# Kernel optimization log

Hardware: AMD Instinct MI355X
Metric: run time of the kernel (lower is better)

Reference implementation:

```python
import jax, jax.numpy as jnp
import numpy as np

B, L, D, C, H, M = 256, 500, 3, 32, 512, 5
I = D + C            # per-step input dim (dihedrals concat condition)
O = D * M            # out_dim * num_mixtures


def setup_inputs() -> dict:
    key = jax.random.key(0)
    ks = jax.random.split(key, 6)
    return {
        "inputs": jax.random.normal(ks[0], (B, L, D), dtype=jnp.float32),
        "z": jax.random.normal(ks[1], (B, L, C), dtype=jnp.float32),
        "W_enc": jax.random.normal(ks[2], (L, I, H), dtype=jnp.float32),
        "b_enc": jnp.zeros((1, H), dtype=jnp.float32),
        "V_mu": jax.random.normal(ks[3], (L, H, O), dtype=jnp.float32),
        "b_mu": jnp.zeros((L, 1, O), dtype=jnp.float32),
        "V_sigma": jax.random.normal(ks[4], (L, H, O), dtype=jnp.float32),
        "b_sigma": jnp.zeros((L, 1, O), dtype=jnp.float32),
        "V_pi": jax.random.normal(ks[5], (L, H, M), dtype=jnp.float32),
        "b_pi": jnp.zeros((L, 1, M), dtype=jnp.float32),
    }


def reference(inputs, z, W_enc, b_enc, V_mu, b_mu, V_sigma, b_sigma, V_pi, b_pi):
    # x: [L, B, I]
    x = jnp.transpose(jnp.concatenate([inputs, z], axis=2), (1, 0, 2))
    # per-step contributions c[i] = x[i] @ W_enc[i] -> [L, B, H]
    c = jnp.einsum('lbi,lih->lbh', x, W_enc)
    # a[i] = b_enc + sum_{j<i} c[j]  (exclusive prefix sum of the recurrence)
    csum = jnp.cumsum(c, axis=0)
    a = jnp.concatenate([jnp.zeros_like(csum[:1]), csum[:-1]], axis=0) + b_enc
    h = jax.nn.relu(a)  # [L, B, H]
    h_mu = jnp.einsum('lbh,lho->lbo', h, V_mu) + b_mu        # [L, B, O]
    h_sigma = jnp.einsum('lbh,lho->lbo', h, V_sigma) + b_sigma
    h_pi = jnp.einsum('lbh,lhm->lbm', h, V_pi) + b_pi        # [L, B, M]
    logits = jnp.concatenate([h_mu, h_sigma, h_pi], axis=2)  # [L, B, 2O+M]
    return jnp.transpose(logits, (1, 0, 2))                  # [B, L, 2O+M]
```

## Files before the change

### kernel.cpp

```cpp
#include <hip/hip_runtime.h>

constexpr int B = 256, L = 500, D = 3, C = 32, I = 35, H = 512, O = 15, M = 5;
constexpr int KP1 = 48;
constexpr int JP = 48;
constexpr int KPV = 520;
constexpr int G = 100;
constexpr int LC = 5;

typedef __attribute__((ext_vector_type(8))) _Float16 half8;
typedef __attribute__((ext_vector_type(2))) _Float16 half2;
typedef __attribute__((ext_vector_type(16))) float f32x16;

__global__ __launch_bounds__(256) void k0x(const float* __restrict__ inp,
                                           const float* __restrict__ z,
                                           _Float16* __restrict__ xT) {
  const int l = blockIdx.x, tid = threadIdx.x;
  __shared__ _Float16 xs[B][38];
  const float* ip = inp + ((size_t)tid * L + l) * D;
  const float4* zp = (const float4*)(z + ((size_t)tid * L + l) * C);
  xs[tid][0] = (_Float16)ip[0];
  xs[tid][1] = (_Float16)ip[1];
  xs[tid][2] = (_Float16)ip[2];
#pragma unroll
  for (int q = 0; q < 8; ++q) {
    float4 v = zp[q];
    xs[tid][D + q * 4 + 0] = (_Float16)v.x;
    xs[tid][D + q * 4 + 1] = (_Float16)v.y;
    xs[tid][D + q * 4 + 2] = (_Float16)v.z;
    xs[tid][D + q * 4 + 3] = (_Float16)v.w;
  }
  __syncthreads();
  unsigned int* dst = (unsigned int*)(xT + (size_t)l * B * KP1);
  for (int f = tid; f < B * (KP1 / 2); f += 256) {
    int b = f / (KP1 / 2), k = (f - b * (KP1 / 2)) * 2;
    unsigned int lo = (k < I)     ? *(const unsigned short*)&xs[b][k]     : 0u;
    unsigned int hi = (k + 1 < I) ? *(const unsigned short*)&xs[b][k + 1] : 0u;
    dst[f] = lo | (hi << 16);
  }
}

__global__ __launch_bounds__(256) void k0w(const float* __restrict__ W,
                                           _Float16* __restrict__ Wt) {
  const int l = blockIdx.x, tid = threadIdx.x;
  __shared__ _Float16 ws[H][37];
  for (int f = tid; f < I * H; f += 256) {
    int i = f >> 9, h = f & 511;
    ws[h][i] = (_Float16)W[((size_t)l * I + i) * H + h];
  }
  __syncthreads();
  unsigned int* dst = (unsigned int*)(Wt + (size_t)l * H * KP1);
  for (int f = tid; f < H * (KP1 / 2); f += 256) {
    int h = f / (KP1 / 2), k = (f - h * (KP1 / 2)) * 2;
    unsigned int lo = (k < I)     ? *(const unsigned short*)&ws[h][k]     : 0u;
    unsigned int hi = (k + 1 < I) ? *(const unsigned short*)&ws[h][k + 1] : 0u;
    dst[f] = lo | (hi << 16);
  }
}

__global__ __launch_bounds__(256) void k0v(const float* __restrict__ Vmu,
                                           const float* __restrict__ Vsg,
                                           const float* __restrict__ Vpi,
                                           _Float16* __restrict__ Vt) {
  const int l = blockIdx.x, tid = threadIdx.x;
  __shared__ __align__(16) _Float16 Vs[JP * KPV];
  for (int f = tid; f < (JP * KPV) / 8; f += 256) ((uint4*)Vs)[f] = (uint4){0, 0, 0, 0};
  __syncthreads();
  const float* vm = Vmu + (size_t)l * H * O;
  const float* vs = Vsg + (size_t)l * H * O;
  const float* vp = Vpi + (size_t)l * H * M;
  for (int idx = tid; idx < H * O; idx += 256) {
    int k = idx / O, j = idx - k * O;
    Vs[j * KPV + k]       = (_Float16)vm[idx];
    Vs[(O + j) * KPV + k] = (_Float16)vs[idx];
  }
  for (int idx = tid; idx < H * M; idx += 256) {
    int k = idx / M, j = idx - k * M;
    Vs[(2 * O + j) * KPV + k] = (_Float16)vp[idx];
  }
  __syncthreads();
  uint4* dst = (uint4*)(Vt + (size_t)l * JP * KPV);
  for (int f = tid; f < (JP * KPV) / 8; f += 256) dst[f] = ((const uint4*)Vs)[f];
}

__global__ __launch_bounds__(256, 3) void kA(const _Float16* __restrict__ xT,
                                             const _Float16* __restrict__ Wt,
                                             _Float16* __restrict__ S) {
  const int idx = blockIdx.x;
  const int g = ((idx >> 6) << 3) + (idx & 7);
  if (g >= G) return;
  const int b0 = ((idx >> 3) & 7) * 32;
  const int w = threadIdx.x >> 6, lane = threadIdx.x & 63;
  const int ln31 = lane & 31, hi32 = lane >> 5;

  f32x16 acc[4];
#pragma unroll
  for (int mt = 0; mt < 4; ++mt)
#pragma unroll
    for (int r = 0; r < 16; ++r) acc[mt][r] = 0.f;

#pragma unroll 1
  for (int t = 0; t < LC; ++t) {
    const int l = g * LC + t;
    const _Float16* Xb = xT + ((size_t)l * B + b0 + ln31) * KP1 + 8 * hi32;
    const _Float16* Wb = Wt + ((size_t)l * H + 128 * w + ln31) * KP1 + 8 * hi32;
    half8 xf[3], wf[12];
#pragma unroll
    for (int kt = 0; kt < 3; ++kt) xf[kt] = *(const half8*)(Xb + 16 * kt);
#pragma unroll
    for (int mt = 0; mt < 4; ++mt)
#pragma unroll
      for (int kt = 0; kt < 3; ++kt)
        wf[mt * 3 + kt] = *(const half8*)(Wb + (size_t)mt * 32 * KP1 + 16 * kt);
#pragma unroll
    for (int mt = 0; mt < 4; ++mt)
#pragma unroll
      for (int kt = 0; kt < 3; ++kt)
        acc[mt] = __builtin_amdgcn_mfma_f32_32x32x16_f16(wf[mt * 3 + kt], xf[kt], acc[mt], 0, 0, 0);
  }
  _Float16* Sp = S + ((size_t)g * H + 128 * w) * B + b0 + ln31;
#pragma unroll
  for (int mt = 0; mt < 4; ++mt)
#pragma unroll
    for (int r = 0; r < 16; ++r) {
      const int hl = 32 * mt + (r & 3) + 8 * (r >> 2) + 4 * hi32;
      Sp[(size_t)hl * B] = (_Float16)acc[mt][r];
    }
}

__global__ __launch_bounds__(256) void kS(const _Float16* __restrict__ S,
                                          const float* __restrict__ benc,
                                          float* __restrict__ Acc) {
  const int t = blockIdx.x * 256 + threadIdx.x;
  const int b = t & (B - 1), h = t >> 8;
  float run = benc[h];
  const _Float16* sp = S + (size_t)h * B + b;
  float* ap = Acc + (size_t)h * B + b;
  constexpr size_t stride = (size_t)H * B;
#pragma unroll 5
  for (int g = 0; g < G; ++g) {
    ap[g * stride] = run;
    run += (float)sp[g * stride];
  }
}

__global__ __launch_bounds__(256, 2) void kB(const _Float16* __restrict__ xT,
                                             const _Float16* __restrict__ Wt,
                                             const _Float16* __restrict__ Vt,
                                             const float* __restrict__ Acc,
                                             const float* __restrict__ bmu,
                                             const float* __restrict__ bsg,
                                             const float* __restrict__ bpi,
                                             float* __restrict__ out) {
  const int idx = blockIdx.x;
  const int g = ((idx >> 6) << 3) + (idx & 7);
  if (g >= G) return;
  const int b0 = ((idx >> 3) & 7) * 32;
  const int tid = threadIdx.x;
  const int w = tid >> 6, lane = tid & 63;
  const int ln31 = lane & 31, hi32 = lane >> 5;

  __shared__ float po[4][32][37];

  f32x16 acc[4];
  const float* Ap = Acc + ((size_t)g * H + 128 * w) * B + b0 + ln31;
#pragma unroll
  for (int mt = 0; mt < 4; ++mt)
#pragma unroll
    for (int r = 0; r < 16; ++r) {
      const int hl = 32 * mt + (r & 3) + 8 * (r >> 2) + 4 * hi32;
      acc[mt][r] = Ap[(size_t)hl * B];
    }

#pragma unroll 1
  for (int t = 0; t < LC; ++t) {
    const int l = g * LC + t;
    const _Float16* Vb = Vt + (size_t)l * JP * KPV + 128 * w + 8 * hi32;
    half8 va0[8];
#pragma unroll
    for (int s = 0; s < 8; ++s)
      va0[s] = *(const half8*)(Vb + 16 * s + (size_t)ln31 * KPV);
    half8 va1[8];
#pragma unroll
    for (int s = 0; s < 8; ++s) {
      va1[s] = half8{};
      if (ln31 < 3)
        va1[s] = *(const half8*)(Vb + 16 * s + (size_t)(32 + ln31) * KPV);
    }
    half8 xf[3], wf[12];
    if (t != LC - 1) {
      const _Float16* Xb = xT + ((size_t)l * B + b0 + ln31) * KP1 + 8 * hi32;
      const _Float16* Wb = Wt + ((size_t)l * H + 128 * w + ln31) * KP1 + 8 * hi32;
#pragma unroll
      for (int kt = 0; kt < 3; ++kt) xf[kt] = *(const half8*)(Xb + 16 * kt);
#pragma unroll
      for (int mt = 0; mt < 4; ++mt)
#pragma unroll
        for (int kt = 0; kt < 3; ++kt)
          wf[mt * 3 + kt] = *(const half8*)(Wb + (size_t)mt * 32 * KP1 + 16 * kt);
    }
    f32x16 o0, o1;
#pragma unroll
    for (int r = 0; r < 16; ++r) { o0[r] = 0.f; o1[r] = 0.f; }
#pragma unroll
    for (int mt = 0; mt < 4; ++mt) {
      unsigned P0[4], P1[4];
#pragma unroll
      for (int m = 0; m < 4; ++m) {
        float e0 = fmaxf(acc[mt][4 * m + 0], 0.f);
        float e1 = fmaxf(acc[mt][4 * m + 1], 0.f);
        float e2 = fmaxf(acc[mt][4 * m + 2], 0.f);
        float e3 = fmaxf(acc[mt][4 * m + 3], 0.f);
        P0[m] = __builtin_bit_cast(unsigned, __builtin_amdgcn_cvt_pkrtz(e0, e1));
        P1[m] = __builtin_bit_cast(unsigned, __builtin_amdgcn_cvt_pkrtz(e2, e3));
      }
#pragma unroll
      for (int tl = 0; tl < 2; ++tl) {
        unsigned w0 = P0[2 * tl], w2 = P0[2 * tl + 1];
        unsigned w1 = P1[2 * tl], w3 = P1[2 * tl + 1];
        asm("v_permlane32_swap_b32 %0, %1" : "+v"(w0), "+v"(w2));
        asm("v_permlane32_swap_b32 %0, %1" : "+v"(w1), "+v"(w3));
        half2 a0 = __builtin_bit_cast(half2, w0);
        half2 a1 = __builtin_bit_cast(half2, w1);
        half2 a2 = __builtin_bit_cast(half2, w2);
        half2 a3 = __builtin_bit_cast(half2, w3);
        half8 hb = {a0.x, a0.y, a1.x, a1.y, a2.x, a2.y, a3.x, a3.y};
        o0 = __builtin_amdgcn_mfma_f32_32x32x16_f16(va0[2 * mt + tl], hb, o0, 0, 0, 0);
        o1 = __builtin_amdgcn_mfma_f32_32x32x16_f16(va1[2 * mt + tl], hb, o1, 0, 0, 0);
      }
    }
    float* pw = &po[w][ln31][0];
#pragma unroll
    for (int r = 0; r < 16; ++r) {
      const int j0 = (r & 3) + 8 * (r >> 2) + 4 * hi32;
      pw[j0] = o0[r];
      if (j0 + 32 < 35) pw[j0 + 32] = o1[r];
    }
    if (t != LC - 1) {
#pragma unroll
      for (int mt = 0; mt < 4; ++mt)
#pragma unroll
        for (int kt = 0; kt < 3; ++kt)
          acc[mt] = __builtin_amdgcn_mfma_f32_32x32x16_f16(wf[mt * 3 + kt], xf[kt], acc[mt], 0, 0, 0);
    }
    __syncthreads();
    for (int f = tid; f < 32 * 35; f += 256) {
      const int b = f / 35, j = f - 35 * b;
      const float s = po[0][b][j] + po[1][b][j] + po[2][b][j] + po[3][b][j];
      const float bias = (j < O) ? bmu[l * O + j]
                       : (j < 2 * O) ? bsg[l * O + (j - O)]
                       : bpi[l * M + (j - 2 * O)];
      out[((size_t)(b0 + b) * L + l) * 35 + j] = s + bias;
    }
    __syncthreads();
  }
}

extern "C" void kernel_launch(void* const* d_in, const int* in_sizes, int n_in,
                              void* d_out, int out_size, void* d_ws, size_t ws_size,
                              hipStream_t stream) {
  const float* inp  = (const float*)d_in[0];
  const float* z    = (const float*)d_in[1];
  const float* Wenc = (const float*)d_in[2];
  const float* benc = (const float*)d_in[3];
  const float* Vmu  = (const float*)d_in[4];
  const float* bmu  = (const float*)d_in[5];
  const float* Vsg  = (const float*)d_in[6];
  const float* bsg  = (const float*)d_in[7];
  const float* Vpi  = (const float*)d_in[8];
  const float* bpi  = (const float*)d_in[9];
  float* out = (float*)d_out;

  char* ws = (char*)d_ws;
  _Float16* xT  = (_Float16*)ws;
  _Float16* Wt  = (_Float16*)(ws + 12288000);
  _Float16* Vt  = (_Float16*)(ws + 36864000);
  _Float16* S   = (_Float16*)(ws + 61824000);
  float*    Acc = (float*)(ws + 88038400);

  k0x<<<dim3(L), 256, 0, stream>>>(inp, z, xT);
  k0w<<<dim3(L), 256, 0, stream>>>(Wenc, Wt);
  k0v<<<dim3(L), 256, 0, stream>>>(Vmu, Vsg, Vpi, Vt);
  kA<<<dim3(832), 256, 0, stream>>>(xT, Wt, S);
  kS<<<dim3(B * H / 256), 256, 0, stream>>>(S, benc, Acc);
  kB<<<dim3(832), 256, 0, stream>>>(xT, Wt, Vt, Acc, bmu, bsg, bpi, out);
}
```

Baseline: 266.4 us.

## Store prefix accumulators in fp16 and batch output epilogue across timesteps

```diff
diff --git a/kernel.cpp b/kernel.cpp
--- a/kernel.cpp
+++ b/kernel.cpp
@@ -129,16 +129,16 @@
 
 __global__ __launch_bounds__(256) void kS(const _Float16* __restrict__ S,
                                           const float* __restrict__ benc,
-                                          float* __restrict__ Acc) {
+                                          _Float16* __restrict__ Acc) {
   const int t = blockIdx.x * 256 + threadIdx.x;
   const int b = t & (B - 1), h = t >> 8;
   float run = benc[h];
   const _Float16* sp = S + (size_t)h * B + b;
-  float* ap = Acc + (size_t)h * B + b;
+  _Float16* ap = Acc + (size_t)h * B + b;
   constexpr size_t stride = (size_t)H * B;
 #pragma unroll 5
   for (int g = 0; g < G; ++g) {
-    ap[g * stride] = run;
+    ap[g * stride] = (_Float16)run;
     run += (float)sp[g * stride];
   }
 }
@@ -146,7 +146,7 @@
 __global__ __launch_bounds__(256, 2) void kB(const _Float16* __restrict__ xT,
                                              const _Float16* __restrict__ Wt,
                                              const _Float16* __restrict__ Vt,
-                                             const float* __restrict__ Acc,
+                                             const _Float16* __restrict__ Acc,
                                              const float* __restrict__ bmu,
                                              const float* __restrict__ bsg,
                                              const float* __restrict__ bpi,
@@ -159,16 +159,24 @@
   const int w = tid >> 6, lane = tid & 63;
   const int ln31 = lane & 31, hi32 = lane >> 5;
 
-  __shared__ float po[4][32][37];
+  __shared__ _Float16 po[4][LC][32][36];
+  __shared__ float bias_s[LC][35];
+
+  if (tid < LC * 35) {
+    const int t = tid / 35, j = tid - 35 * t, l = g * LC + t;
+    bias_s[t][j] = (j < O) ? bmu[l * O + j]
+                 : (j < 2 * O) ? bsg[l * O + (j - O)]
+                 : bpi[l * M + (j - 2 * O)];
+  }
 
   f32x16 acc[4];
-  const float* Ap = Acc + ((size_t)g * H + 128 * w) * B + b0 + ln31;
+  const _Float16* Ap = Acc + ((size_t)g * H + 128 * w) * B + b0 + ln31;
 #pragma unroll
   for (int mt = 0; mt < 4; ++mt)
 #pragma unroll
     for (int r = 0; r < 16; ++r) {
       const int hl = 32 * mt + (r & 3) + 8 * (r >> 2) + 4 * hi32;
-      acc[mt][r] = Ap[(size_t)hl * B];
+      acc[mt][r] = (float)Ap[(size_t)hl * B];
     }
 
 #pragma unroll 1
@@ -228,12 +236,17 @@
         o1 = __builtin_amdgcn_mfma_f32_32x32x16_f16(va1[2 * mt + tl], hb, o1, 0, 0, 0);
       }
     }
-    float* pw = &po[w][ln31][0];
-#pragma unroll
-    for (int r = 0; r < 16; ++r) {
+    _Float16* pw = &po[w][t][ln31][0];
+#pragma unroll
+    for (int r = 0; r < 16; r += 2) {
       const int j0 = (r & 3) + 8 * (r >> 2) + 4 * hi32;
-      pw[j0] = o0[r];
-      if (j0 + 32 < 35) pw[j0 + 32] = o1[r];
+      *(unsigned*)&pw[j0] =
+          __builtin_bit_cast(unsigned, __builtin_amdgcn_cvt_pkrtz(o0[r], o0[r + 1]));
+    }
+    if (hi32 == 0) {
+      *(unsigned*)&pw[32] =
+          __builtin_bit_cast(unsigned, __builtin_amdgcn_cvt_pkrtz(o1[0], o1[1]));
+      pw[34] = (_Float16)o1[2];
     }
     if (t != LC - 1) {
 #pragma unroll
@@ -242,16 +255,15 @@
         for (int kt = 0; kt < 3; ++kt)
           acc[mt] = __builtin_amdgcn_mfma_f32_32x32x16_f16(wf[mt * 3 + kt], xf[kt], acc[mt], 0, 0, 0);
     }
-    __syncthreads();
-    for (int f = tid; f < 32 * 35; f += 256) {
-      const int b = f / 35, j = f - 35 * b;
-      const float s = po[0][b][j] + po[1][b][j] + po[2][b][j] + po[3][b][j];
-      const float bias = (j < O) ? bmu[l * O + j]
-                       : (j < 2 * O) ? bsg[l * O + (j - O)]
-                       : bpi[l * M + (j - 2 * O)];
-      out[((size_t)(b0 + b) * L + l) * 35 + j] = s + bias;
-    }
-    __syncthreads();
+  }
+  __syncthreads();
+  for (int f = tid; f < 32 * LC * 35; f += 256) {
+    const int b = f / (LC * 35);
+    const int r = f - b * (LC * 35);
+    const int t = r / 35, j = r - 35 * t;
+    const float s = (float)po[0][t][b][j] + (float)po[1][t][b][j] +
+                    (float)po[2][t][b][j] + (float)po[3][t][b][j];
+    out[((size_t)(b0 + b) * L + g * LC + t) * 35 + j] = s + bias_s[t][j];
   }
 }
 
@@ -275,7 +287,7 @@
   _Float16* Wt  = (_Float16*)(ws + 12288000);
   _Float16* Vt  = (_Float16*)(ws + 36864000);
   _Float16* S   = (_Float16*)(ws + 61824000);
-  float*    Acc = (float*)(ws + 88038400);
+  _Float16* Acc = (_Float16*)(ws + 88038400);
 
   k0x<<<dim3(L), 256, 0, stream>>>(inp, z, xT);
   k0w<<<dim3(L), 256, 0, stream>>>(Wenc, Wt);
```

New measurement: 252.2 us. -5.3%, faster.
